# Optimization experiments

Measured on AMD Instinct MI355X. Metric: run time of the kernel, lower is better.

Reference implementation:

```python
import jax, jax.numpy as jnp
import numpy as np


def _seg_softmax(z, seg, num_seg):
    # PyG-style softmax over segments (numerically stable)
    m = jax.ops.segment_max(z, seg, num_segments=num_seg)
    e = jnp.exp(z - m[seg])
    s = jax.ops.segment_sum(e, seg, num_segments=num_seg)
    return e / s[seg]


def _structure(x, W, b, edge_index, batch):
    """Eager (numpy) watershed structure: peaks + level-synchronous BFS fill.
    Faithful to Clusterer.forward/fill: peaks are nodes whose elevation >= all
    in-neighbors; BFS expands along descending edges, a node joins the
    cluster(s) of whichever frontier origins reach it first (ties -> all),
    and is never re-assigned afterwards. Index structure is non-differentiable
    (matches torch autograd semantics)."""
    x = np.asarray(x); W = np.asarray(W); b = np.asarray(b)
    ei = np.asarray(edge_index); batch = np.asarray(batch)
    N = x.shape[0]; B = int(batch.max()) + 1
    # elevation = softmax(Linear(x), batch)
    z = (x @ W.T).ravel() + b[0]
    m = np.full(B, -np.inf, dtype=np.float64); np.maximum.at(m, batch, z)
    e = np.exp(z - m[batch]); s = np.zeros(B); np.add.at(s, batch, e)
    elev = e / s[batch]
    src, dst = ei[0], ei[1]
    # peaks: every incoming edge (src->dst) has elev[dst] >= elev[src]
    deg = np.bincount(dst, minlength=N)
    ge = np.bincount(dst[elev[dst] >= elev[src]], minlength=N)
    peaks = np.nonzero(ge == deg)[0]  # sorted, includes isolated nodes
    # descending edges only
    dmask = elev[dst] <= elev[src]
    ds, dd = src[dmask], dst[dmask]
    mems_list = [peaks]; ids_list = [peaks]
    visited = np.zeros(N, dtype=bool); visited[peaks] = True
    fn, fc = peaks, peaks  # frontier (node, cluster-id) pairs
    while fn.size:
        order = np.argsort(fn, kind='stable')
        fcs = fc[order]
        counts = np.bincount(fn, minlength=N)
        starts = np.concatenate([np.zeros(1, np.int64), np.cumsum(counts)])
        emask = counts[ds] > 0
        es, ed = ds[emask], dd[emask]
        rep = counts[es]
        tot = int(rep.sum())
        if tot == 0:
            break
        # attribute each descent edge to every cluster id of its origin
        base = np.repeat(starts[es], rep)
        grp = np.cumsum(rep) - rep
        within = np.arange(tot) - np.repeat(grp, rep)
        nc = fcs[base + within]
        nd = np.repeat(ed, rep)
        keep = ~visited[nd]  # nodes already in a cluster are never re-assigned
        nd, nc = nd[keep], nc[keep]
        if nd.size == 0:
            break
        pairs = np.unique(np.stack([nd, nc], axis=1), axis=0)
        nd, nc = pairs[:, 0], pairs[:, 1]
        visited[nd] = True
        mems_list.append(nd); ids_list.append(nc)
        fn, fc = nd, nc
    mems = np.concatenate(mems_list)
    ids = np.concatenate(ids_list)
    new_ids = np.searchsorted(peaks, ids)  # relabel peak node ids -> 0..P-1
    cluster_batch = batch[peaks]
    return mems, new_ids, peaks, cluster_batch, int(peaks.size), B


def setup_inputs() -> dict:
    rng = np.random.default_rng(0)
    N, C, B = 100000, 256, 8
    Ng = N // B
    Eu = 800000  # undirected edge draws, ~avg degree 16 after symmetrization
    g = rng.integers(0, B, Eu)
    s = g * Ng + rng.integers(0, Ng, Eu)
    d = g * Ng + rng.integers(0, Ng, Eu)
    keep = s != d
    s, d = s[keep], d[keep]
    src = np.concatenate([s, d]); dst = np.concatenate([d, s])
    key = src * N + dst
    _, idx = np.unique(key, return_index=True)  # coalesce (sorted, deduped)
    edge_index = np.stack([src[idx], dst[idx]]).astype(np.int64)
    batch = np.repeat(np.arange(B), Ng).astype(np.int64)
    x = rng.standard_normal((N, C)).astype(np.float32)
    W = (rng.standard_normal((1, C)) * 0.05).astype(np.float32)
    b = np.zeros((1,), np.float32)
    return {"x": jnp.asarray(x), "edge_index": jnp.asarray(edge_index),
            "batch": jnp.asarray(batch), "W": jnp.asarray(W), "b": jnp.asarray(b)}


def reference(x, edge_index, batch, W, b):
    mems, ids, peaks, cbatch, P, B = _structure(x, W, b, edge_index, batch)
    mems_j = jnp.asarray(mems); ids_j = jnp.asarray(ids); cb = jnp.asarray(cbatch)
    # differentiable pooling math (TopoPool.get_elevations + TopoPool.scale)
    z = (x @ W.T)[:, 0] + b[0]                       # [N]
    elev = _seg_softmax(z, batch, B)                  # per-graph softmax
    max_elev = jax.ops.segment_max(elev[mems_j], ids_j, num_segments=P)   # [P]
    max_x = jax.ops.segment_max(x[mems_j], ids_j, num_segments=P)        # [P,C]
    normed = _seg_softmax(max_elev, cb, B)            # softmax over clusters per graph
    pooled = max_x * normed[:, None]                  # [P,C]
    return pooled, cb, elev
```

## Files before the change

### kernel.cpp

```cpp
#include <hip/hip_runtime.h>
#include <hip/hip_bf16.h>
#include <stdint.h>


#define LINF 0x3FFFFFFF
#define MAXL 60
#define LSPLIT 10
#define NGMAX 12544
#define TAILCAP 8192

__device__ __forceinline__ unsigned encf(float f) {
  unsigned u = __float_as_uint(f);
  return (u & 0x80000000u) ? ~u : (u | 0x80000000u);
}
__device__ __forceinline__ float decf(unsigned u) {
  unsigned v = (u & 0x80000000u) ? (u & 0x7fffffffu) : ~u;
  return __uint_as_float(v);
}
__device__ __forceinline__ float bf2f(unsigned h) {
  return __uint_as_float(h << 16);
}
__device__ __forceinline__ unsigned f2bf(float f) {
  unsigned u = __float_as_uint(f);
  return (u + 0x7FFFu + ((u >> 16) & 1u)) >> 16;
}

__global__ void k_z(const float* __restrict__ x, const float* __restrict__ W,
                    const float* __restrict__ b, const int* __restrict__ batch,
                    float* __restrict__ z, unsigned* __restrict__ bmax_enc,
                    unsigned short* __restrict__ M, int N, int C) {
  __shared__ unsigned smax[8];
  if (threadIdx.x < 8) smax[threadIdx.x] = 0u;
  __syncthreads();
  int lane = threadIdx.x & 63;
  int wid = threadIdx.x >> 6;
  int chunk = (N + gridDim.x - 1) / gridDim.x;
  int v0 = blockIdx.x * chunk;
  int v1 = min(v0 + chunk, N);
  float b0 = b[0];
  for (int v = v0 + (wid << 2); v < v1; v += 16) {
    int nv = min(4, v1 - v);
    float acc[4] = {0.f, 0.f, 0.f, 0.f};
    for (int f = lane * 4; f < C; f += 256) {
      float4 xv[4];
      #pragma unroll
      for (int k = 0; k < 4; ++k) {
        int vv = v + (k < nv ? k : 0);
        xv[k] = *(const float4*)(x + (size_t)vv * C + f);
      }
      float4 wv = *(const float4*)(W + f);
      #pragma unroll
      for (int k = 0; k < 4; ++k) {
        acc[k] += xv[k].x * wv.x + xv[k].y * wv.y + xv[k].z * wv.z + xv[k].w * wv.w;
      }
      #pragma unroll
      for (int k = 0; k < 4; ++k) {
        if (k < nv) {
          uint2 pk;
          pk.x = f2bf(xv[k].x) | (f2bf(xv[k].y) << 16);
          pk.y = f2bf(xv[k].z) | (f2bf(xv[k].w) << 16);
          *(uint2*)(M + (size_t)(v + k) * C + f) = pk;
        }
      }
    }
    #pragma unroll
    for (int off = 32; off > 0; off >>= 1) {
      acc[0] += __shfl_xor(acc[0], off, 64);
      acc[1] += __shfl_xor(acc[1], off, 64);
      acc[2] += __shfl_xor(acc[2], off, 64);
      acc[3] += __shfl_xor(acc[3], off, 64);
    }
    if (lane < nv) {
      float zv = acc[lane] + b0;
      z[v + lane] = zv;
      atomicMax(&smax[batch[v + lane] & 7], encf(zv));
    }
  }
  __syncthreads();
  if (threadIdx.x < 8)
    if (smax[threadIdx.x]) atomicMax(&bmax_enc[threadIdx.x], smax[threadIdx.x]);
}

__global__ void k_e(const float* __restrict__ z, const int* __restrict__ batch,
                    const unsigned* __restrict__ bmax_enc, float* __restrict__ e,
                    float* __restrict__ bsum, int N) {
  __shared__ float ssum[1024];
  for (int i = threadIdx.x; i < 1024; i += blockDim.x) ssum[i] = 0.f;
  __syncthreads();
  int i = blockIdx.x * blockDim.x + threadIdx.x;
  if (i < N) {
    int bt = batch[i] & 1023;
    float ev = expf(z[i] - decf(bmax_enc[bt]));
    e[i] = ev;
    atomicAdd(&ssum[bt], ev);
  }
  __syncthreads();
  for (int t = threadIdx.x; t < 1024; t += blockDim.x)
    if (ssum[t] != 0.f) atomicAdd(&bsum[t], ssum[t]);
}

__global__ void k_edges(const int* __restrict__ ei, const float* __restrict__ z,
                        int* __restrict__ notpeak, int* __restrict__ desc_cnt,
                        const float* __restrict__ e, const float* __restrict__ bsum,
                        const int* __restrict__ batch, float* __restrict__ elev_out,
                        int E, int N) {
  int i = blockIdx.x * blockDim.x + threadIdx.x;
  if (i < N) elev_out[i] = e[i] / bsum[batch[i] & 1023];
  if (i >= E) return;
  int s = ei[i], d = ei[E + i];
  float zs = z[s], zd = z[d];
  if (zd < zs) notpeak[d] = 1;
  if (zd <= zs) atomicAdd(&desc_cnt[s], 1);
}

__global__ void k_chunksum2(const int* __restrict__ desc_cnt, const int* __restrict__ notpeak,
                            int n, int* __restrict__ csA, int* __restrict__ csB) {
  __shared__ int sA[512], sB[512];
  int t = threadIdx.x;
  int i = blockIdx.x * 512 + t;
  int a = 0, bb = 0;
  if (i < n) { a = desc_cnt[i]; bb = (notpeak[i] == 0) ? 1 : 0; }
  sA[t] = a; sB[t] = bb;
  __syncthreads();
  for (int off = 256; off > 0; off >>= 1) {
    if (t < off) { sA[t] += sA[t + off]; sB[t] += sB[t + off]; }
    __syncthreads();
  }
  if (t == 0) { csA[blockIdx.x] = sA[0]; csB[blockIdx.x] = sB[0]; }
}

__global__ void k_chunkscan2(int* __restrict__ csA, int* __restrict__ csB, int nchunks) {
  __shared__ int sA[1024], sB[1024];
  int t = threadIdx.x;
  int vA = (t < nchunks) ? csA[t] : 0;
  int vB = (t < nchunks) ? csB[t] : 0;
  sA[t] = vA; sB[t] = vB;
  __syncthreads();
  for (int off = 1; off < 1024; off <<= 1) {
    int aA = (t >= off) ? sA[t - off] : 0;
    int aB = (t >= off) ? sB[t - off] : 0;
    __syncthreads();
    sA[t] += aA; sB[t] += aB;
    __syncthreads();
  }
  if (t < nchunks) { csA[t] = sA[t] - vA; csB[t] = sB[t] - vB; }
}

__global__ void k_offsets(const int* __restrict__ vals, const int* __restrict__ chunkoff,
                          int2* __restrict__ ocp, int* __restrict__ cursor, int n) {
  __shared__ int s[512];
  int t = threadIdx.x;
  int i = blockIdx.x * 512 + t;
  int v = (i < n) ? vals[i] : 0;
  s[t] = v;
  __syncthreads();
  for (int off = 1; off < 512; off <<= 1) {
    int add = (t >= off) ? s[t - off] : 0;
    __syncthreads();
    s[t] += add;
    __syncthreads();
  }
  if (i < n) {
    int excl = s[t] - v + chunkoff[blockIdx.x];
    ocp[i] = make_int2(excl, excl);
    cursor[i] = excl;
  }
}

__global__ void k_peak_emit(const int* __restrict__ notpeak, const int* __restrict__ chunkoff,
                            const int* __restrict__ batch, const float* __restrict__ elev,
                            int* __restrict__ peaklist, int* __restrict__ cbatch,
                            float* __restrict__ out_cb, float* __restrict__ melev,
                            int n, int P) {
  __shared__ int s[512];
  int t = threadIdx.x;
  int i = blockIdx.x * 512 + t;
  int v = (i < n) ? (notpeak[i] == 0 ? 1 : 0) : 0;
  s[t] = v;
  __syncthreads();
  for (int off = 1; off < 512; off <<= 1) {
    int add = (t >= off) ? s[t - off] : 0;
    __syncthreads();
    s[t] += add;
    __syncthreads();
  }
  if (i < n && v) {
    int r = s[t] - 1 + chunkoff[blockIdx.x];
    if (r < P) {
      peaklist[r] = i;
      int bt = batch[i];
      cbatch[r] = bt;
      out_cb[r] = (float)bt;
      melev[r] = elev[i];
    }
  }
}

__global__ void k_fill(const int* __restrict__ ei, const float* __restrict__ z,
                       int* __restrict__ cursor, int* __restrict__ adj, int E) {
  int i = blockIdx.x * blockDim.x + threadIdx.x;
  if (i >= E) return;
  int s = ei[i], d = ei[E + i];
  if (z[d] <= z[s]) {
    int pos = atomicAdd(&cursor[s], 1);
    adj[pos] = d;
  }
}

__global__ void __launch_bounds__(1024, 1)
k_levels(const int* __restrict__ adj, const int2* __restrict__ ocp,
         const int* __restrict__ desc_cnt, const int* __restrict__ notpeak,
         int* __restrict__ level, int* __restrict__ lnodes,
         int* __restrict__ qend_g, int Ng, int N) {
  __shared__ int lvl[NGMAX];
  __shared__ unsigned short lq[NGMAX];
  __shared__ int soff[NGMAX + 1];
  __shared__ int s_qe;
  __shared__ int qend_s[64];
  const int b = blockIdx.x, base = b * Ng;
  const int tid = threadIdx.x, nth = blockDim.x;

  if (tid == 0) s_qe = 0;
  __syncthreads();
  for (int i = tid; i < Ng; i += nth) {
    soff[i] = ocp[base + i].x;
    bool pk = (notpeak[base + i] == 0);
    lvl[i] = pk ? 0 : LINF;
    if (pk) { int p = atomicAdd(&s_qe, 1); lq[p] = (unsigned short)i; }
  }
  if (tid == 0)
    soff[Ng] = (base + Ng < N) ? ocp[base + Ng].x : (ocp[N - 1].x + desc_cnt[N - 1]);
  __syncthreads();
  int qb = 0, qe = s_qe;
  int L = 0;
  while (L < MAXL && qe > qb) {
    if (tid == 0) qend_s[L] = qe;
    int units = (qe - qb) << 2;
    for (int t = tid; t < units; t += nth) {
      int qi = qb + (t >> 2), sub = t & 3;
      int lu = (int)lq[qi];
      int o = soff[lu], oe = soff[lu + 1];
      int j = o + sub;
      if (j < oe) {
        int w0 = adj[j];
        for (;;) {
          int jn = j + 4;
          int w1 = (jn < oe) ? adj[jn] : 0;
          int wl = w0 - base;
          if (lvl[wl] == LINF) {
            int old = atomicMin(&lvl[wl], L + 1);
            if (old == LINF) { int p = atomicAdd(&s_qe, 1); lq[p] = (unsigned short)wl; }
          }
          if (jn >= oe) break;
          w0 = w1; j = jn;
        }
      }
    }
    __syncthreads();
    int nq = s_qe;
    __syncthreads();
    qb = qe; qe = nq; ++L;
  }
  if (tid == 0) {
    for (int l = L; l < 63; ++l) qend_s[l] = qe;
    qend_s[63] = L;
  }
  __syncthreads();
  if (tid < 64) qend_g[b * 64 + tid] = qend_s[tid];
  for (int i = tid; i < Ng; i += nth) level[base + i] = lvl[i];
  for (int qi = tid; qi < qe; qi += nth) lnodes[base + qi] = (int)lq[qi];
}

__global__ void k_filter(const int* __restrict__ ei, const float* __restrict__ z,
                         const int* __restrict__ level, int2* __restrict__ ocp,
                         int* __restrict__ adj, int E) {
  int i = blockIdx.x * blockDim.x + threadIdx.x;
  if (i >= E) return;
  int s = ei[i], d = ei[E + i];
  if (z[d] <= z[s] && level[d] == level[s] + 1) {
    int pos = atomicAdd(&ocp[s].y, 1);
    adj[pos] = d;
  }
}

__global__ void __launch_bounds__(1024, 1)
k_dp_deep(const int* __restrict__ lnodes, const int* __restrict__ qend_g,
          const int2* __restrict__ ocp, const int* __restrict__ adj,
          unsigned short* __restrict__ M, int Ng, int C) {
  __shared__ unsigned short lqd[TAILCAP];
  __shared__ int2 soc[TAILCAP];
  __shared__ int qend_s[64];
  const int b = blockIdx.x, base = b * Ng;
  const int tid = threadIdx.x, nth = blockDim.x;
  if (tid < 64) qend_s[tid] = qend_g[b * 64 + tid];
  __syncthreads();
  const int Lmax = qend_s[63];
  if (Lmax - 1 < LSPLIT) return;
  const int ts = qend_s[LSPLIT - 1];
  const int qe = qend_s[62];
  const int tn = qe - ts;
  const bool useCache = (tn > 0) && (tn <= TAILCAP);
  if (useCache) {
    for (int i = tid; i < tn; i += nth) {
      int lid = lnodes[base + ts + i];
      lqd[i] = (unsigned short)lid;
      soc[i] = ocp[base + lid];
    }
  }
  __syncthreads();
  const int lane = tid & 31, hw = tid >> 5, nhw = nth >> 5;
  for (int L2 = Lmax - 1; L2 >= LSPLIT; --L2) {
    int sL = qend_s[L2 - 1], eL = qend_s[L2];
    for (int p = sL + hw; p < eL; p += nhw) {
      int u, o, e2;
      if (useCache) { u = base + (int)lqd[p - ts]; int2 v = soc[p - ts]; o = v.x; e2 = v.y; }
      else          { int lid = lnodes[base + p]; u = base + lid; int2 v = ocp[u]; o = v.x; e2 = v.y; }
      if (e2 == o) continue;
      uint4 sq = ((const uint4*)(M + (size_t)u * C))[lane];
      float4 a0, a1;
      a0.x = bf2f(sq.x & 0xffffu); a0.y = bf2f(sq.x >> 16);
      a0.z = bf2f(sq.y & 0xffffu); a0.w = bf2f(sq.y >> 16);
      a1.x = bf2f(sq.z & 0xffffu); a1.y = bf2f(sq.z >> 16);
      a1.z = bf2f(sq.w & 0xffffu); a1.w = bf2f(sq.w >> 16);
      for (int j = o; j < e2; ++j) {
        int wn = adj[j];
        uint4 q = ((const uint4*)(M + (size_t)wn * C))[lane];
        a0.x = fmaxf(a0.x, bf2f(q.x & 0xffffu));
        a0.y = fmaxf(a0.y, bf2f(q.x >> 16));
        a0.z = fmaxf(a0.z, bf2f(q.y & 0xffffu));
        a0.w = fmaxf(a0.w, bf2f(q.y >> 16));
        a1.x = fmaxf(a1.x, bf2f(q.z & 0xffffu));
        a1.y = fmaxf(a1.y, bf2f(q.z >> 16));
        a1.z = fmaxf(a1.z, bf2f(q.w & 0xffffu));
        a1.w = fmaxf(a1.w, bf2f(q.w >> 16));
      }
      uint4 pk4;
      pk4.x = f2bf(a0.x) | (f2bf(a0.y) << 16);
      pk4.y = f2bf(a0.z) | (f2bf(a0.w) << 16);
      pk4.z = f2bf(a1.x) | (f2bf(a1.y) << 16);
      pk4.w = f2bf(a1.z) | (f2bf(a1.w) << 16);
      ((uint4*)(M + (size_t)u * C))[lane] = pk4;
    }
    __syncthreads();
  }
}

__global__ void __launch_bounds__(256)
k_dp(const int* __restrict__ lnodes, const int* __restrict__ qend,
     const int* __restrict__ adj, const int2* __restrict__ ocp,
     unsigned short* __restrict__ M, int L, int C, int Ng) {
  const int b = blockIdx.y;
  int lane = threadIdx.x & 31;
  int ghw = (blockIdx.x * blockDim.x + threadIdx.x) >> 5;
  int nhw = (gridDim.x * blockDim.x) >> 5;
  int s = L ? qend[b * 64 + L - 1] : 0;
  int e = qend[b * 64 + L];
  for (int idx = s + ghw; idx < e; idx += nhw) {
    int u = b * Ng + lnodes[b * Ng + idx];
    int2 oc2 = ocp[u];
    int o = oc2.x, oc = oc2.y - oc2.x;
    if (oc == 0) continue;
    uint4 sq = ((const uint4*)(M + (size_t)u * C))[lane];
    float4 a0, a1;
    a0.x = bf2f(sq.x & 0xffffu); a0.y = bf2f(sq.x >> 16);
    a0.z = bf2f(sq.y & 0xffffu); a0.w = bf2f(sq.y >> 16);
    a1.x = bf2f(sq.z & 0xffffu); a1.y = bf2f(sq.z >> 16);
    a1.z = bf2f(sq.w & 0xffffu); a1.w = bf2f(sq.w >> 16);
    for (int j = 0; j < oc; j += 4) {
      int m = oc - j;
      int wn[4];
      #pragma unroll
      for (int k = 0; k < 4; k++) wn[k] = adj[o + j + (k < m ? k : 0)];
      #pragma unroll
      for (int k = 0; k < 4; k++) {
        uint4 q = ((const uint4*)(M + (size_t)wn[k] * C))[lane];
        a0.x = fmaxf(a0.x, bf2f(q.x & 0xffffu));
        a0.y = fmaxf(a0.y, bf2f(q.x >> 16));
        a0.z = fmaxf(a0.z, bf2f(q.y & 0xffffu));
        a0.w = fmaxf(a0.w, bf2f(q.y >> 16));
        a1.x = fmaxf(a1.x, bf2f(q.z & 0xffffu));
        a1.y = fmaxf(a1.y, bf2f(q.z >> 16));
        a1.z = fmaxf(a1.z, bf2f(q.w & 0xffffu));
        a1.w = fmaxf(a1.w, bf2f(q.w >> 16));
      }
    }
    uint4 p;
    p.x = f2bf(a0.x) | (f2bf(a0.y) << 16);
    p.y = f2bf(a0.z) | (f2bf(a0.w) << 16);
    p.z = f2bf(a1.x) | (f2bf(a1.y) << 16);
    p.w = f2bf(a1.z) | (f2bf(a1.w) << 16);
    ((uint4*)(M + (size_t)u * C))[lane] = p;
  }
}

__global__ void k_cnorm(const float* __restrict__ melev, const int* __restrict__ cbatch,
                        float* __restrict__ normed, int P) {
  __shared__ unsigned cm[1024];
  __shared__ float cs[1024];
  int t = threadIdx.x;
  for (int i = t; i < 1024; i += blockDim.x) { cm[i] = 0u; cs[i] = 0.f; }
  __syncthreads();
  for (int i = t; i < P; i += blockDim.x) atomicMax(&cm[cbatch[i] & 1023], encf(melev[i]));
  __syncthreads();
  for (int i = t; i < P; i += blockDim.x) {
    int bt = cbatch[i] & 1023;
    atomicAdd(&cs[bt], expf(melev[i] - decf(cm[bt])));
  }
  __syncthreads();
  for (int i = t; i < P; i += blockDim.x) {
    int bt = cbatch[i] & 1023;
    normed[i] = expf(melev[i] - decf(cm[bt])) / cs[bt];
  }
}

__global__ void __launch_bounds__(256)
k_dp0_pool(const int* __restrict__ peaklist, const float* __restrict__ normed,
           const int* __restrict__ adj, const int2* __restrict__ ocp,
           const unsigned short* __restrict__ M, float* __restrict__ out,
           int P, int C) {
  int lane = threadIdx.x & 31;
  int ghw = (blockIdx.x * blockDim.x + threadIdx.x) >> 5;
  int nhw = (gridDim.x * blockDim.x) >> 5;
  for (int r = ghw; r < P; r += nhw) {
    int u = peaklist[r];
    int2 oc2 = ocp[u];
    int o = oc2.x, oc = oc2.y - oc2.x;
    uint4 sq = ((const uint4*)(M + (size_t)u * C))[lane];
    float4 a0, a1;
    a0.x = bf2f(sq.x & 0xffffu); a0.y = bf2f(sq.x >> 16);
    a0.z = bf2f(sq.y & 0xffffu); a0.w = bf2f(sq.y >> 16);
    a1.x = bf2f(sq.z & 0xffffu); a1.y = bf2f(sq.z >> 16);
    a1.z = bf2f(sq.w & 0xffffu); a1.w = bf2f(sq.w >> 16);
    for (int j = 0; j < oc; j += 4) {
      int m = oc - j;
      int wn[4];
      #pragma unroll
      for (int k = 0; k < 4; k++) wn[k] = adj[o + j + (k < m ? k : 0)];
      #pragma unroll
      for (int k = 0; k < 4; k++) {
        uint4 q = ((const uint4*)(M + (size_t)wn[k] * C))[lane];
        a0.x = fmaxf(a0.x, bf2f(q.x & 0xffffu));
        a0.y = fmaxf(a0.y, bf2f(q.x >> 16));
        a0.z = fmaxf(a0.z, bf2f(q.y & 0xffffu));
        a0.w = fmaxf(a0.w, bf2f(q.y >> 16));
        a1.x = fmaxf(a1.x, bf2f(q.z & 0xffffu));
        a1.y = fmaxf(a1.y, bf2f(q.z >> 16));
        a1.z = fmaxf(a1.z, bf2f(q.w & 0xffffu));
        a1.w = fmaxf(a1.w, bf2f(q.w >> 16));
      }
    }
    float nr = normed[r];
    float* orow = out + (size_t)r * C + lane * 8;
    float4 o0 = make_float4(a0.x * nr, a0.y * nr, a0.z * nr, a0.w * nr);
    float4 o1 = make_float4(a1.x * nr, a1.y * nr, a1.z * nr, a1.w * nr);
    ((float4*)orow)[0] = o0;
    ((float4*)orow)[1] = o1;
  }
}

extern "C" void kernel_launch(void* const* d_in, const int* in_sizes, int n_in,
                              void* d_out, int out_size, void* d_ws, size_t ws_size,
                              hipStream_t stream) {
  const float* x = (const float*)d_in[0];
  const int* ei = (const int*)d_in[1];
  const int* batch = (const int*)d_in[2];
  const float* W = (const float*)d_in[3];
  const float* b = (const float*)d_in[4];

  const int N = in_sizes[2];
  const int C = in_sizes[0] / N;
  const int E = in_sizes[1] / 2;
  const int P = (out_size - N) / (C + 1);
  const int B = 8;
  const int Ng = N / B;

  float* out = (float*)d_out;
  float* out_pooled = out;
  float* out_cb = out + (size_t)P * C;
  float* out_elev = out_cb + P;

  char* w = (char*)d_ws;
  size_t off = 0;
  auto alloc = [&](size_t bytes) -> void* {
    off = (off + 255) & ~(size_t)255;
    void* p = (void*)(w + off);
    off += bytes;
    return p;
  };
  size_t zero_begin = 0;
  int* notpeak      = (int*)alloc((size_t)N * 4);
  int* desc_cnt     = (int*)alloc((size_t)N * 4);
  unsigned* bmax    = (unsigned*)alloc(1024 * 4);
  float* bsum       = (float*)alloc(1024 * 4);
  size_t zero_end = off;
  float* z          = (float*)alloc((size_t)N * 4);
  float* e          = (float*)alloc((size_t)N * 4);
  int2* ocp         = (int2*)alloc((size_t)N * 8);
  int* cursor       = (int*)alloc((size_t)N * 4);
  int* level        = (int*)alloc((size_t)N * 4);
  int* lnodes       = (int*)alloc((size_t)N * 4);
  int* qend         = (int*)alloc((size_t)B * 64 * 4);
  const int nchunks = (N + 511) / 512;
  int* csA          = (int*)alloc((size_t)nchunks * 4);
  int* csB          = (int*)alloc((size_t)nchunks * 4);
  int* cbatch       = (int*)alloc((size_t)P * 4);
  float* normed     = (float*)alloc((size_t)P * 4);
  float* melev      = (float*)alloc((size_t)P * 4);
  int* peaklist     = (int*)alloc((size_t)P * 4);
  int* adj          = (int*)alloc((size_t)E * 4);
  unsigned short* M = (unsigned short*)alloc((size_t)N * C * 2);

  hipMemsetAsync(w + zero_begin, 0, zero_end - zero_begin, stream);

  k_z<<<2048, 256, 0, stream>>>(x, W, b, batch, z, bmax, M, N, C);
  int nblkN = (N + 255) / 256;
  k_e<<<nblkN, 256, 0, stream>>>(z, batch, bmax, e, bsum, N);
  int nblkE = (E + 255) / 256;
  k_edges<<<nblkE, 256, 0, stream>>>(ei, z, notpeak, desc_cnt, e, bsum, batch,
                                     out_elev, E, N);
  k_chunksum2<<<nchunks, 512, 0, stream>>>(desc_cnt, notpeak, N, csA, csB);
  k_chunkscan2<<<1, 1024, 0, stream>>>(csA, csB, nchunks);
  k_offsets<<<nchunks, 512, 0, stream>>>(desc_cnt, csA, ocp, cursor, N);
  k_fill<<<nblkE, 256, 0, stream>>>(ei, z, cursor, adj, E);
  k_peak_emit<<<nchunks, 512, 0, stream>>>(notpeak, csB, batch, out_elev,
                                           peaklist, cbatch, out_cb, melev, N, P);
  k_cnorm<<<1, 1024, 0, stream>>>(melev, cbatch, normed, P);
  k_levels<<<B, 1024, 0, stream>>>(adj, ocp, desc_cnt, notpeak, level, lnodes,
                                   qend, Ng, N);
  k_filter<<<nblkE, 256, 0, stream>>>(ei, z, level, ocp, adj, E);
  k_dp_deep<<<B, 1024, 0, stream>>>(lnodes, qend, ocp, adj, M, Ng, C);
  dim3 gdp(256, B);
  for (int L = LSPLIT - 1; L >= 1; --L) {
    k_dp<<<gdp, 256, 0, stream>>>(lnodes, qend, adj, ocp, M, L, C, Ng);
  }
  k_dp0_pool<<<512, 256, 0, stream>>>(peaklist, normed, adj, ocp, M, out_pooled,
                                      P, C);
}
```

Baseline: 508.9 us.

## Replace queue-based BFS with level-scan BFS and post-hoc counting sort of nodes

The per-graph BFS kernel no longer keeps an explicit frontier queue built with shared atomics. Each level now scans all nodes and expands those at the current level, marking neighbours with plain stores and a per-level any flag. Level boundaries and the level-ordered node list are then rebuilt afterwards with a histogram, a wavefront prefix scan and a scatter. This removes atomicMin and queue atomics from the hot loop, but every level now scans all Ng nodes and the four-way per-node edge split is gone, which may cost more when graphs have many levels.

Result: slower. 650.6 us (+27.8%).

```diff
diff --git a/kernel.cpp b/kernel.cpp
--- a/kernel.cpp
+++ b/kernel.cpp
@@ -213,62 +213,66 @@
          int* __restrict__ level, int* __restrict__ lnodes,
          int* __restrict__ qend_g, int Ng, int N) {
   __shared__ int lvl[NGMAX];
-  __shared__ unsigned short lq[NGMAX];
   __shared__ int soff[NGMAX + 1];
-  __shared__ int s_qe;
-  __shared__ int qend_s[64];
+  __shared__ int s_any[MAXL + 2];
+  __shared__ int s_cnt[64];
   const int b = blockIdx.x, base = b * Ng;
   const int tid = threadIdx.x, nth = blockDim.x;
 
-  if (tid == 0) s_qe = 0;
-  __syncthreads();
+  for (int l = tid; l < MAXL + 2; l += nth) s_any[l] = 0;
+  for (int l = tid; l < 64; l += nth) s_cnt[l] = 0;
   for (int i = tid; i < Ng; i += nth) {
     soff[i] = ocp[base + i].x;
     bool pk = (notpeak[base + i] == 0);
     lvl[i] = pk ? 0 : LINF;
-    if (pk) { int p = atomicAdd(&s_qe, 1); lq[p] = (unsigned short)i; }
+    if (pk) s_any[0] = 1;
   }
   if (tid == 0)
     soff[Ng] = (base + Ng < N) ? ocp[base + Ng].x : (ocp[N - 1].x + desc_cnt[N - 1]);
   __syncthreads();
-  int qb = 0, qe = s_qe;
   int L = 0;
-  while (L < MAXL && qe > qb) {
-    if (tid == 0) qend_s[L] = qe;
-    int units = (qe - qb) << 2;
-    for (int t = tid; t < units; t += nth) {
-      int qi = qb + (t >> 2), sub = t & 3;
-      int lu = (int)lq[qi];
-      int o = soff[lu], oe = soff[lu + 1];
-      int j = o + sub;
-      if (j < oe) {
-        int w0 = adj[j];
-        for (;;) {
-          int jn = j + 4;
-          int w1 = (jn < oe) ? adj[jn] : 0;
-          int wl = w0 - base;
+  while (L < MAXL && s_any[L]) {
+    for (int i = tid; i < Ng; i += nth) {
+      if (lvl[i] == L) {
+        int o = soff[i], oe = soff[i + 1];
+        for (int j = o; j < oe; ++j) {
+          int wl = adj[j] - base;
           if (lvl[wl] == LINF) {
-            int old = atomicMin(&lvl[wl], L + 1);
-            if (old == LINF) { int p = atomicAdd(&s_qe, 1); lq[p] = (unsigned short)wl; }
+            lvl[wl] = L + 1;
+            s_any[L + 1] = 1;
           }
-          if (jn >= oe) break;
-          w0 = w1; j = jn;
         }
       }
     }
     __syncthreads();
-    int nq = s_qe;
-    __syncthreads();
-    qb = qe; qe = nq; ++L;
-  }
-  if (tid == 0) {
-    for (int l = L; l < 63; ++l) qend_s[l] = qe;
-    qend_s[63] = L;
-  }
-  __syncthreads();
-  if (tid < 64) qend_g[b * 64 + tid] = qend_s[tid];
-  for (int i = tid; i < Ng; i += nth) level[base + i] = lvl[i];
-  for (int qi = tid; qi < qe; qi += nth) lnodes[base + qi] = (int)lq[qi];
+    ++L;
+  }
+  const int Lmax = L;
+  for (int i = tid; i < Ng; i += nth) {
+    int lv = lvl[i];
+    level[base + i] = lv;
+    if (lv != LINF) atomicAdd(&s_cnt[lv], 1);
+  }
+  __syncthreads();
+  if (tid < 64) {
+    int v = s_cnt[tid];
+    int inc = v;
+    #pragma unroll
+    for (int o2 = 1; o2 < 64; o2 <<= 1) {
+      int t2 = __shfl_up(inc, o2, 64);
+      if (tid >= o2) inc += t2;
+    }
+    qend_g[b * 64 + tid] = (tid == 63) ? Lmax : inc;
+    s_cnt[tid] = inc - v;
+  }
+  __syncthreads();
+  for (int i = tid; i < Ng; i += nth) {
+    int lv = lvl[i];
+    if (lv != LINF) {
+      int pos = atomicAdd(&s_cnt[lv], 1);
+      lnodes[base + pos] = i;
+    }
+  }
 }
 
 __global__ void k_filter(const int* __restrict__ ei, const float* __restrict__ z,
```
